# Optimization experiments

Hardware: AMD Instinct MI355X
Metric: run time of the kernel (lower is better)

Reference implementation:

```python
import jax, jax.numpy as jnp
import numpy as np
from jax import lax

WEIGHT_BITS = 8
ACT_BITS = 8
EPS = 1e-8


def ste_round(x):
    # straight-through estimator round
    return x + lax.stop_gradient(jnp.round(x) - x)


def fq_sym(x, bits=WEIGHT_BITS):
    # symmetric per-tensor signed fake quant (Brevitas Int*PerTensorFloat style)
    n = 2.0 ** (bits - 1) - 1.0
    scale = lax.stop_gradient(jnp.maximum(jnp.max(jnp.abs(x)), EPS) / n)
    return jnp.clip(ste_round(x / scale), -n, n) * scale


def quant_relu(x, bits=ACT_BITS):
    # QuantReLU: relu then unsigned per-tensor fake quant
    n = 2.0 ** bits - 1.0
    y = jax.nn.relu(x)
    scale = lax.stop_gradient(jnp.maximum(jnp.max(y), EPS) / n)
    return jnp.clip(ste_round(y / scale), 0.0, n) * scale


def qconv(x, w, b, groups=1):
    # QuantConv2d: fake-quant weights & bias, then conv (stride 1, same padding)
    pad = w.shape[-1] // 2
    wq = fq_sym(w, WEIGHT_BITS)
    bq = fq_sym(b, WEIGHT_BITS)
    y = lax.conv_general_dilated(
        x, wq, window_strides=(1, 1), padding=[(pad, pad), (pad, pad)],
        dimension_numbers=('NCHW', 'OIHW', 'NCHW'), feature_group_count=groups)
    return y + bq[None, :, None, None]


def residual_dw(x, w, b):
    # Residual(depthwise conv -> QuantReLU) with QuantIdentity(ActQuant) on both branches
    C = x.shape[1]
    h = quant_relu(qconv(x, w, b, groups=C))
    return fq_sym(h, ACT_BITS) + fq_sym(x, ACT_BITS)


def setup_inputs() -> dict:
    key = jax.random.key(0)
    ks = jax.random.split(key, 11)
    B, C, H, W = 8, 128, 128, 128
    CO = 256
    s = 0.05
    return {
        'x': jax.random.normal(ks[0], (B, C, H, W), jnp.float32),
        'dw1_w': jax.random.normal(ks[1], (C, 1, 3, 3), jnp.float32) * s,
        'dw1_b': jax.random.normal(ks[2], (C,), jnp.float32) * s,
        'dw2_w': jax.random.normal(ks[3], (C, 1, 3, 3), jnp.float32) * s,
        'dw2_b': jax.random.normal(ks[4], (C,), jnp.float32) * s,
        'pw1_w': jax.random.normal(ks[5], (4 * C, C, 1, 1), jnp.float32) * s,
        'pw1_b': jax.random.normal(ks[6], (4 * C,), jnp.float32) * s,
        'pw2_w': jax.random.normal(ks[7], (C, 4 * C, 1, 1), jnp.float32) * s,
        'pw2_b': jax.random.normal(ks[8], (C,), jnp.float32) * s,
        'up_w': jax.random.normal(ks[9], (CO, C, 3, 3), jnp.float32) * s,
        'up_b': jax.random.normal(ks[10], (CO,), jnp.float32) * s,
    }


def reference(x, dw1_w, dw1_b, dw2_w, dw2_b, pw1_w, pw1_b, pw2_w, pw2_b, up_w, up_b):
    # depth=1 block
    h = residual_dw(x, dw1_w, dw1_b)
    h = residual_dw(h, dw2_w, dw2_b)
    h = quant_relu(qconv(h, pw1_w, pw1_b))       # 1x1 expand C -> 4C
    h = quant_relu(qconv(h, pw2_w, pw2_b))       # 1x1 contract 4C -> C
    h = quant_relu(qconv(h, up_w, up_b))         # ConvBlock 3x3 C -> ch_out
    return h
```

## Files before the change

### kernel.cpp

```cpp
#include <hip/hip_runtime.h>

#define EPSQ 1e-8f

typedef unsigned short u16;
typedef signed char i8;
typedef __attribute__((ext_vector_type(4))) int int4v;
typedef __attribute__((ext_vector_type(4))) unsigned int uint4v;

static constexpr int  Bn = 8, Cc = 128, Hh = 128, Ww = 128, HW = Hh * Ww;
static constexpr int  C4 = 512, CO = 256;
static constexpr long NX   = (long)Bn * Cc * HW;
static constexpr long NOUT = (long)Bn * CO * HW;

#define MFMAI8(a,b,c) __builtin_amdgcn_mfma_i32_16x16x64_i8(a,b,c,0,0,0)

__device__ __forceinline__ float ubits(unsigned u) { return __uint_as_float(u); }


__device__ __forceinline__ void block_max_atomic(float v, unsigned* slot) {
    #pragma unroll
    for (int off = 32; off; off >>= 1) v = fmaxf(v, __shfl_down(v, off));
    __shared__ float sm[8];
    int lane = threadIdx.x & 63, wid = threadIdx.x >> 6;
    if (lane == 0) sm[wid] = v;
    __syncthreads();
    if (threadIdx.x == 0) {
        float m = sm[0];
        int nw = (blockDim.x + 63) >> 6;
        for (int i = 1; i < nw; i++) m = fmaxf(m, sm[i]);
        if (m > __uint_as_float(*(volatile unsigned*)slot))
            atomicMax(slot, __float_as_uint(m));
    }
    __syncthreads();
}

__device__ __forceinline__ void block_max_atomic2(float v, unsigned* slot, float* sm) {
    #pragma unroll
    for (int off = 32; off; off >>= 1) v = fmaxf(v, __shfl_down(v, off));
    int lane = threadIdx.x & 63, wid = threadIdx.x >> 6;
    __syncthreads();
    if (lane == 0) sm[wid] = v;
    __syncthreads();
    if (threadIdx.x == 0) {
        float m = sm[0];
        int nw = (blockDim.x + 63) >> 6;
        for (int i = 1; i < nw; i++) m = fmaxf(m, sm[i]);
        if (m > __uint_as_float(*(volatile unsigned*)slot))
            atomicMax(slot, __float_as_uint(m));
    }
}


__global__ void absmax_kernel(const float* __restrict__ x, long n, unsigned* slot) {
    long i = (long)blockIdx.x * blockDim.x + threadIdx.x;
    long stride = (long)gridDim.x * blockDim.x;
    const float4* x4 = (const float4*)x;
    long n4 = n >> 2;
    float m = 0.f;
    for (long j = i; j < n4; j += stride) {
        float4 v = x4[j];
        m = fmaxf(m, fmaxf(fmaxf(fabsf(v.x), fabsf(v.y)), fmaxf(fabsf(v.z), fabsf(v.w))));
    }
    block_max_atomic(m, slot);
}

struct QW { const float* src; float* dstF; i8* dstC; int n; int mode; int slot; int kdim; };

__device__ __forceinline__ QW qw_select(const QW& q0, const QW& q1, const QW& q2, const QW& q3,
                                        const QW& q4, const QW& q5, const QW& q6, const QW& q7,
                                        const QW& q8, const QW& q9, int t) {
    switch (t) {
        case 0: return q0; case 1: return q1; case 2: return q2; case 3: return q3;
        case 4: return q4; case 5: return q5; case 6: return q6; case 7: return q7;
        case 8: return q8; default: return q9;
    }
}

__global__ void wabsmax_kernel(QW q0, QW q1, QW q2, QW q3, QW q4,
                               QW q5, QW q6, QW q7, QW q8, QW q9,
                               unsigned* __restrict__ scal) {
    QW q = qw_select(q0, q1, q2, q3, q4, q5, q6, q7, q8, q9, blockIdx.y);
    int i0 = blockIdx.x * blockDim.x + threadIdx.x;
    int str = gridDim.x * blockDim.x;
    float m = 0.f;
    for (int i = i0; i < q.n; i += str) m = fmaxf(m, fabsf(q.src[i]));
    block_max_atomic(m, scal + 16 + blockIdx.y);
}

__global__ void wquant_kernel(QW q0, QW q1, QW q2, QW q3, QW q4,
                              QW q5, QW q6, QW q7, QW q8, QW q9,
                              unsigned* __restrict__ scal) {
    QW q = qw_select(q0, q1, q2, q3, q4, q5, q6, q7, q8, q9, blockIdx.y);
    float s = fmaxf(ubits(scal[16 + blockIdx.y]), EPSQ) / 127.f;
    if (q.mode != 0 && blockIdx.x == 0 && threadIdx.x == 0) scal[q.slot] = __float_as_uint(s);
    int i0 = blockIdx.x * blockDim.x + threadIdx.x;
    int str = gridDim.x * blockDim.x;
    for (int i = i0; i < q.n; i += str) {
        float v = fminf(fmaxf(rintf(q.src[i] / s), -127.f), 127.f);
        int code = (int)v;
        if (q.mode == 0) q.dstF[i] = v * s;
        else if (q.mode == 1) {
            int o = i / q.kdim, k = i % q.kdim;
            int otile = o >> 4, r = o & 15, kb = k >> 6, qq = (k & 63) >> 4, e = k & 15;
            q.dstC[((otile * (q.kdim >> 6) + kb) * 64 + qq * 16 + r) * 16 + e] = (i8)code;
        } else {
            int o = i / 1152, rem = i % 1152, c = rem / 9, t = rem % 9;
            int otile = o >> 4, r = o & 15, kb = c >> 6, qq = (c & 63) >> 4, e = c & 15;
            q.dstC[(((otile * 9 + t) * 2 + kb) * 64 + qq * 16 + r) * 16 + e] = (i8)code;
        }
    }
}


__global__ void corr_kernel(const float* __restrict__ pw2_w, const float* __restrict__ up_w,
                            const unsigned* __restrict__ scal,
                            int* __restrict__ corrP2, int* __restrict__ corrU) {
    int lane = threadIdx.x;
    if (blockIdx.y == 0) {
        int o = blockIdx.x;
        if (o >= 128) return;
        float s = fmaxf(ubits(scal[16 + 6]), EPSQ) / 127.f;
        int sum = 0;
        for (int k = lane; k < 512; k += 64)
            sum += (int)fminf(fmaxf(rintf(pw2_w[o * 512 + k] / s), -127.f), 127.f);
        #pragma unroll
        for (int off = 32; off; off >>= 1) sum += __shfl_down(sum, off);
        if (lane == 0) corrP2[o] = sum;
    } else {
        int o = blockIdx.x;
        float s = fmaxf(ubits(scal[16 + 8]), EPSQ) / 127.f;
        int sum[3] = {0, 0, 0};
        for (int i = lane; i < 1152; i += 64) {
            int t = i % 9;
            int code = (int)fminf(fmaxf(rintf(up_w[o * 1152 + i] / s), -127.f), 127.f);
            sum[t / 3] += code;
        }
        #pragma unroll
        for (int r = 0; r < 3; r++) {
            int v = sum[r];
            #pragma unroll
            for (int off = 32; off; off >>= 1) v += __shfl_down(v, off);
            if (lane == 0) corrU[r * 256 + o] = v;
        }
    }
}


__global__ void dwconv_kernel(const float* __restrict__ in, const float* __restrict__ wq,
                              const float* __restrict__ bq, float* __restrict__ out,
                              unsigned* mslot) {
    int bc = blockIdx.x;
    int c  = bc & (Cc - 1);
    float w[9];
    #pragma unroll
    for (int k = 0; k < 9; k++) w[k] = wq[c * 9 + k];
    float bias = bq[c];
    const float* src = in + (long)bc * HW;
    float* dst = out + (long)bc * HW;
    int j  = threadIdx.x & (Ww - 1);
    int r2 = threadIdx.x >> 7;
    float mm = 0.f;
    #pragma unroll
    for (int rr = 0; rr < 4; rr++) {
        int i = blockIdx.y * 8 + rr * 2 + r2;
        float acc = 0.f;
        #pragma unroll
        for (int di = 0; di < 3; di++) {
            int ii = i + di - 1;
            if (ii < 0 || ii >= Hh) continue;
            #pragma unroll
            for (int dj = 0; dj < 3; dj++) {
                int jj = j + dj - 1;
                if (jj < 0 || jj >= Ww) continue;
                acc = fmaf(w[di * 3 + dj], src[ii * Ww + jj], acc);
            }
        }
        acc += bias;
        dst[i * Ww + j] = acc;
        mm = fmaxf(mm, fmaxf(acc, 0.f));
    }
    block_max_atomic(mm, mslot);
}


__global__ void residual_kernel(const float4* __restrict__ t, const float4* __restrict__ xin,
                                float4* __restrict__ r, const unsigned* __restrict__ scal,
                                int mReluIdx, int mXIdx, unsigned* mOut) {
    float s1  = fmaxf(__uint_as_float(scal[mReluIdx]), EPSQ) / 255.f;
    float mh  = 255.f * s1;
    float s1b = fmaxf(mh, EPSQ) / 127.f;
    float sx  = fmaxf(__uint_as_float(scal[mXIdx]), EPSQ) / 127.f;
    long i0 = (long)blockIdx.x * blockDim.x + threadIdx.x;
    long str = (long)gridDim.x * blockDim.x;
    long n4 = NX >> 2;
    float mm = 0.f;
    for (long i = i0; i < n4; i += str) {
        float4 tv = t[i];
        float4 xv = xin[i];
        float o[4];
        float tc[4] = {tv.x, tv.y, tv.z, tv.w};
        float xc[4] = {xv.x, xv.y, xv.z, xv.w};
        #pragma unroll
        for (int k = 0; k < 4; k++) {
            float h  = fminf(rintf(fmaxf(tc[k], 0.f) / s1), 255.f) * s1;
            float hq = fminf(fmaxf(rintf(h / s1b), -127.f), 127.f) * s1b;
            float xq = fminf(fmaxf(rintf(xc[k] / sx), -127.f), 127.f) * sx;
            o[k] = hq + xq;
            mm = fmaxf(mm, fabsf(o[k]));
        }
        float4 ov = {o[0], o[1], o[2], o[3]};
        r[i] = ov;
    }
    if (mOut) block_max_atomic(mm, mOut);
}


__global__ __launch_bounds__(256) void residual2_codes_kernel(
    const float* __restrict__ t2, const float* __restrict__ r1,
    i8* __restrict__ jc, i8* __restrict__ ic, const unsigned* __restrict__ scal) {
    float s1  = fmaxf(ubits(scal[3]), EPSQ) / 255.f;
    float s1b = fmaxf(255.f * s1, EPSQ) / 127.f;
    float sx  = fmaxf(ubits(scal[2]), EPSQ) / 127.f;
    int b = blockIdx.x >> 8;
    long px0 = (long)(blockIdx.x & 255) * 64;
    __shared__ __align__(16) i8 lj[64 * 128];
    __shared__ __align__(16) i8 li[64 * 128];
    int px = threadIdx.x & 63, cq = threadIdx.x >> 6;
    for (int it = 0; it < 8; it++) {
        int cb = it * 16 + cq * 4;
        unsigned pj = 0, pi = 0;
        #pragma unroll
        for (int e = 0; e < 4; e++) {
            int c = cb + e;
            long g = ((long)b * Cc + c) * HW + px0 + px;
            float t = t2[g], x = r1[g];
            float hq = fminf(rintf(fmaxf(t, 0.f) / s1), 255.f) * s1;
            int j = (int)fminf(fmaxf(rintf(hq / s1b), -127.f), 127.f);
            int i = (int)fminf(fmaxf(rintf(x / sx), -127.f), 127.f);
            pj |= ((unsigned)(unsigned char)(i8)j) << (8 * e);
            pi |= ((unsigned)(unsigned char)(i8)i) << (8 * e);
        }
        int ad = (px * 128 + cb) ^ ((px & 7) << 4);
        *reinterpret_cast<int*>(lj + ad) = (int)pj;
        *reinterpret_cast<int*>(li + ad) = (int)pi;
    }
    __syncthreads();
    for (int s = threadIdx.x; s < 512; s += 256) {
        int px2 = s >> 3, sl = s & 7;
        int ad = (px2 * 128 + sl * 16) ^ ((px2 & 7) << 4);
        long dst = ((long)b * HW + px0 + px2) * 128 + sl * 16;
        *reinterpret_cast<uint4v*>(jc + dst) = *reinterpret_cast<uint4v*>(lj + ad);
        *reinterpret_cast<uint4v*>(ic + dst) = *reinterpret_cast<uint4v*>(li + ad);
    }
}

template<int K, int OB, bool DUAL, int MODE>
__global__ __launch_bounds__(256) void pwmfma_kernel(
    const i8* __restrict__ bc0, const i8* __restrict__ bc1,
    const i8* __restrict__ wc, const float* __restrict__ bias,
    i8* __restrict__ outc, const unsigned* __restrict__ scal,
    const int* __restrict__ corrI,
    int O_total, int sInSlot, int sWSlot, int sOutSlot, unsigned* mslot) {

    constexpr int F = OB / 64;
    constexpr int KB = K / 64;
    constexpr int LSZ = (DUAL ? 2 : 1) * 64 * K;
    __shared__ __align__(16) i8 lds[LSZ];
    int lane = threadIdx.x & 63, wv = threadIdx.x >> 6;
    int lane15 = lane & 15;
    int b = blockIdx.x >> 8;
    long px0 = (long)(blockIdx.x & 255) * 64;
    long pixbase = (long)b * HW + px0;
    int oB = blockIdx.y * OB;
    int oW = wv * (OB / 4);

    for (int s = threadIdx.x; s < 4 * K; s += 256) {
        int px = s / (K / 16), cs = s % (K / 16);
        long gsrc = (pixbase + px) * K + cs * 16;
        int addr = (px * K + cs * 16) ^ ((px & 7) << 4);
        *reinterpret_cast<uint4v*>(lds + addr) = *reinterpret_cast<const uint4v*>(bc0 + gsrc);
        if (DUAL)
            *reinterpret_cast<uint4v*>(lds + 64 * K + addr) =
                *reinterpret_cast<const uint4v*>(bc1 + gsrc);
    }
    __syncthreads();

    const int4v z4 = {0, 0, 0, 0};
    int4v accA[F][4], accB[F][4];
    #pragma unroll
    for (int i = 0; i < F; i++)
        #pragma unroll
        for (int j = 0; j < 4; j++) { accA[i][j] = z4; accB[i][j] = z4; }

    const i8* wpack = wc + ((long)((oB + oW) >> 4) * KB) * 1024 + lane * 16;

    #pragma unroll
    for (int kb = 0; kb < KB; kb++) {
        int4v a[F];
        #pragma unroll
        for (int f = 0; f < F; f++)
            a[f] = *reinterpret_cast<const int4v*>(wpack + ((long)f * KB + kb) * 1024);
        #pragma unroll
        for (int fn = 0; fn < 4; fn++) {
            int col = fn * 16 + lane15;
            int ad = (col * K + kb * 64 + (lane >> 4) * 16) ^ ((col & 7) << 4);
            int4v b0 = *reinterpret_cast<const int4v*>(lds + ad);
            #pragma unroll
            for (int f = 0; f < F; f++) accA[f][fn] = MFMAI8(a[f], b0, accA[f][fn]);
            if (DUAL) {
                int4v b1 = *reinterpret_cast<const int4v*>(lds + 64 * K + ad);
                #pragma unroll
                for (int f = 0; f < F; f++) accB[f][fn] = MFMAI8(a[f], b1, accB[f][fn]);
            }
        }
    }

    float sW = ubits(scal[sWSlot]);
    float sA, sB_;
    if (DUAL) {
        float s1 = fmaxf(ubits(scal[3]), EPSQ) / 255.f;
        sA  = fmaxf(255.f * s1, EPSQ) / 127.f;
        sB_ = fmaxf(ubits(scal[2]), EPSQ) / 127.f;
    } else {
        sA = fmaxf(ubits(scal[sInSlot]), EPSQ) / 255.f;
        sB_ = 0.f;
    }

    if (MODE == 0) {
        float mm = 0.f;
        #pragma unroll
        for (int f = 0; f < F; f++)
        #pragma unroll
        for (int fn = 0; fn < 4; fn++)
        #pragma unroll
        for (int r = 0; r < 4; r++) {
            int o = oB + oW + f * 16 + (lane >> 4) * 4 + r;
            float av;
            if (DUAL) av = sA * (float)accA[f][fn][r] + sB_ * (float)accB[f][fn][r];
            else      av = sA * (float)(accA[f][fn][r] + (corrI[o] << 7));
            float v = fmaxf(sW * av + bias[o], 0.f);
            mm = fmaxf(mm, v);
        }
        block_max_atomic2(mm, mslot, reinterpret_cast<float*>(lds));
    } else {
        float sOut = fmaxf(ubits(scal[sOutSlot]), EPSQ) / 255.f;
        __syncthreads();
        #pragma unroll
        for (int f = 0; f < F; f++)
        #pragma unroll
        for (int fn = 0; fn < 4; fn++) {
            int orow0 = oW + f * 16 + (lane >> 4) * 4;
            unsigned pk = 0;
            #pragma unroll
            for (int r = 0; r < 4; r++) {
                int o = oB + orow0 + r;
                float av;
                if (DUAL) av = sA * (float)accA[f][fn][r] + sB_ * (float)accB[f][fn][r];
                else      av = sA * (float)(accA[f][fn][r] + (corrI[o] << 7));
                float v = fmaxf(sW * av + bias[o], 0.f);
                int code = (int)fminf(rintf(v / sOut), 255.f) - 128;
                pk |= ((unsigned)(unsigned char)(i8)code) << (8 * r);
            }
            int pxl = fn * 16 + lane15;
            int ad = (pxl * OB + orow0) ^ ((pxl & 7) << 4);
            *reinterpret_cast<int*>(lds + ad) = (int)pk;
        }
        __syncthreads();
        constexpr int CH = OB / 16;
        for (int s = threadIdx.x; s < 64 * CH; s += 256) {
            int px = s / CH, sl = s % CH;
            int ad = (px * OB + sl * 16) ^ ((px & 7) << 4);
            *reinterpret_cast<uint4v*>(outc + (pixbase + px) * O_total + oB + sl * 16) =
                *reinterpret_cast<uint4v*>(lds + ad);
        }
    }
}


__global__ __launch_bounds__(256) void conv3x3_mfma_kernel(
    const i8* __restrict__ xc,
    const i8* __restrict__ wc,
    const float* __restrict__ bias, float* __restrict__ out,
    const unsigned* __restrict__ scal, const int* __restrict__ corrU,
    unsigned* mslot) {

    __shared__ __align__(16) i8 lds[3 * 66 * 128];
    int lane = threadIdx.x & 63, wv = threadIdx.x >> 6;
    int lane15 = lane & 15;
    int bx = blockIdx.x;
    int b = bx >> 8, h = (bx >> 1) & 127, wseg = bx & 1;
    int oW = wv * 64;

    for (int s = threadIdx.x; s < 3 * 66 * 8; s += 256) {
        int row = s / (66 * 8), rem = s % (66 * 8), col = rem >> 3, sl = rem & 7;
        int hh = h + row - 1;
        if (hh < 0 || hh > 127) continue;
        int wgl = wseg * 64 + col - 1;
        uint4v v = {0x80808080u, 0x80808080u, 0x80808080u, 0x80808080u};
        if (wgl >= 0 && wgl <= 127) {
            long pix = (long)b * HW + (long)hh * 128 + wgl;
            v = *reinterpret_cast<const uint4v*>(xc + pix * 128 + sl * 16);
        }
        int addr = ((row * 66 + col) * 128 + sl * 16) ^ ((col & 7) << 4);
        *reinterpret_cast<uint4v*>(lds + addr) = v;
    }
    __syncthreads();

    const int4v z4 = {0, 0, 0, 0};
    int4v acc[4][4];
    #pragma unroll
    for (int i = 0; i < 4; i++)
        #pragma unroll
        for (int j = 0; j < 4; j++) acc[i][j] = z4;

    const i8* wpack = wc + (long)(wv * 4) * 18 * 1024 + lane * 16;
    for (int di = 0; di < 3; di++) {
        int hh = h + di - 1;
        if (hh < 0 || hh > 127) continue;
        for (int dj = 0; dj < 3; dj++) {
            int tap = di * 3 + dj;
            #pragma unroll
            for (int kb = 0; kb < 2; kb++) {
                int4v a[4];
                #pragma unroll
                for (int f = 0; f < 4; f++)
                    a[f] = *reinterpret_cast<const int4v*>(
                        wpack + ((long)(f * 9 + tap) * 2 + kb) * 1024);
                int4v bb[4];
                #pragma unroll
                for (int fn = 0; fn < 4; fn++) {
                    int col = fn * 16 + lane15 + dj;
                    bb[fn] = *reinterpret_cast<const int4v*>(lds +
                        (((di * 66 + col) * 128 + kb * 64 + (lane >> 4) * 16) ^ ((col & 7) << 4)));
                }
                #pragma unroll
                for (int f = 0; f < 4; f++)
                    #pragma unroll
                    for (int fn = 0; fn < 4; fn++)
                        acc[f][fn] = MFMAI8(a[f], bb[fn], acc[f][fn]);
            }
        }
    }

    float s5 = fmaxf(ubits(scal[5]), EPSQ) / 255.f;
    float sc = ubits(scal[10]) * s5;
    float mm = 0.f;
    #pragma unroll
    for (int f = 0; f < 4; f++)
    #pragma unroll
    for (int r = 0; r < 4; r++) {
        int o = oW + f * 16 + (lane >> 4) * 4 + r;
        int csum = corrU[256 + o];
        if (h > 0)   csum += corrU[o];
        if (h < 127) csum += corrU[512 + o];
        #pragma unroll
        for (int fn = 0; fn < 4; fn++) {
            int px = wseg * 64 + fn * 16 + lane15;
            int ai = acc[f][fn][r] + (csum << 7);
            float v = fmaxf(sc * (float)ai + bias[o], 0.f);
            mm = fmaxf(mm, v);
            out[((long)(b * CO + o)) * HW + h * 128 + px] = v;
        }
    }
    block_max_atomic2(mm, mslot, reinterpret_cast<float*>(lds));
}


__global__ void quant_inplace_kernel(float4* __restrict__ p, long n4,
                                     const unsigned* __restrict__ scal, int idx) {
    float s = fmaxf(__uint_as_float(scal[idx]), EPSQ) / 255.f;
    long i0 = (long)blockIdx.x * blockDim.x + threadIdx.x;
    long str = (long)gridDim.x * blockDim.x;
    for (long i = i0; i < n4; i += str) {
        float4 v = p[i];
        v.x = fminf(rintf(v.x / s), 255.f) * s;
        v.y = fminf(rintf(v.y / s), 255.f) * s;
        v.z = fminf(rintf(v.z / s), 255.f) * s;
        v.w = fminf(rintf(v.w / s), 255.f) * s;
        p[i] = v;
    }
}


extern "C" void kernel_launch(void* const* d_in, const int* in_sizes, int n_in,
                              void* d_out, int out_size, void* d_ws, size_t ws_size,
                              hipStream_t stream) {
    (void)in_sizes; (void)n_in; (void)out_size; (void)ws_size;
    const float* x     = (const float*)d_in[0];
    const float* dw1_w = (const float*)d_in[1];
    const float* dw1_b = (const float*)d_in[2];
    const float* dw2_w = (const float*)d_in[3];
    const float* dw2_b = (const float*)d_in[4];
    const float* pw1_w = (const float*)d_in[5];
    const float* pw1_b = (const float*)d_in[6];
    const float* pw2_w = (const float*)d_in[7];
    const float* pw2_b = (const float*)d_in[8];
    const float* up_w  = (const float*)d_in[9];
    const float* up_b  = (const float*)d_in[10];
    float* out = (float*)d_out;
    float* ws  = (float*)d_ws;

    float* Abuf = ws;
    float* Bbuf = ws + NX;
    i8*    jcode   = (i8*)(ws + 2 * NX);
    i8*    icode   = jcode + NX;
    i8*    p1codes = (i8*)ws;
    i8*    p2codes = (i8*)(ws + 2 * NX);

    float* wbase  = ws + 3 * NX;
    float* wq_dw1 = wbase;          float* bq_dw1 = wbase + 1152;
    float* wq_dw2 = wbase + 1280;   float* bq_dw2 = wbase + 2432;
    float* bq_pw1 = wbase + 2560;
    float* bq_pw2 = wbase + 3072;
    float* bq_up  = wbase + 3200;
    i8*    wc_pw1 = (i8*)(wbase + 3456);
    i8*    wc_pw2 = (i8*)(wbase + 19840);
    i8*    wc_up  = (i8*)(wbase + 36224);
    unsigned* scal = (unsigned*)(wbase + 109952);
    int*   corrU  = (int*)(wbase + 109984);
    int*   corrP2 = (int*)(wbase + 110752);

    (void)hipMemsetAsync(scal, 0, 32 * sizeof(unsigned), stream);

    QW q0{dw1_w, wq_dw1, nullptr, 1152, 0, 0, 9},
       q1{dw1_b, bq_dw1, nullptr, 128, 0, 0, 1},
       q2{dw2_w, wq_dw2, nullptr, 1152, 0, 0, 9},
       q3{dw2_b, bq_dw2, nullptr, 128, 0, 0, 1},
       q4{pw1_w, nullptr, wc_pw1, 65536, 1, 8, 128},
       q5{pw1_b, bq_pw1, nullptr, 512, 0, 0, 1},
       q6{pw2_w, nullptr, wc_pw2, 65536, 1, 9, 512},
       q7{pw2_b, bq_pw2, nullptr, 128, 0, 0, 1},
       q8{up_w, nullptr, wc_up, 294912, 2, 10, 128},
       q9{up_b, bq_up, nullptr, 256, 0, 0, 1};
    wabsmax_kernel<<<dim3(32, 10), 256, 0, stream>>>(q0, q1, q2, q3, q4, q5, q6, q7, q8, q9, scal);
    wquant_kernel<<<dim3(32, 10), 256, 0, stream>>>(q0, q1, q2, q3, q4, q5, q6, q7, q8, q9, scal);
    corr_kernel<<<dim3(256, 2), 64, 0, stream>>>(pw2_w, up_w, scal, corrP2, corrU);

    absmax_kernel<<<2048, 256, 0, stream>>>(x, NX, scal + 0);

    dwconv_kernel<<<dim3(Bn * Cc, Hh / 8), 256, 0, stream>>>(x, wq_dw1, bq_dw1, Abuf, scal + 1);
    residual_kernel<<<4096, 256, 0, stream>>>((const float4*)Abuf, (const float4*)x,
                                              (float4*)Bbuf, scal, 1, 0, scal + 2);
    dwconv_kernel<<<dim3(Bn * Cc, Hh / 8), 256, 0, stream>>>(Bbuf, wq_dw2, bq_dw2, Abuf, scal + 3);
    residual2_codes_kernel<<<2048, 256, 0, stream>>>(Abuf, Bbuf, jcode, icode, scal);

    pwmfma_kernel<128, 256, true, 0><<<dim3(2048, 2), 256, 0, stream>>>(
        jcode, icode, wc_pw1, bq_pw1, nullptr, scal, nullptr, C4, 0, 8, 0, scal + 4);
    pwmfma_kernel<128, 256, true, 1><<<dim3(2048, 2), 256, 0, stream>>>(
        jcode, icode, wc_pw1, bq_pw1, p1codes, scal, nullptr, C4, 0, 8, 4, nullptr);

    pwmfma_kernel<512, 128, false, 0><<<dim3(2048, 1), 256, 0, stream>>>(
        p1codes, nullptr, wc_pw2, bq_pw2, nullptr, scal, corrP2, Cc, 4, 9, 0, scal + 5);
    pwmfma_kernel<512, 128, false, 1><<<dim3(2048, 1), 256, 0, stream>>>(
        p1codes, nullptr, wc_pw2, bq_pw2, p2codes, scal, corrP2, Cc, 4, 9, 5, nullptr);

    conv3x3_mfma_kernel<<<2048, 256, 0, stream>>>(p2codes, wc_up, bq_up, out, scal, corrU, scal + 6);
    quant_inplace_kernel<<<4096, 256, 0, stream>>>((float4*)out, NOUT / 4, scal, 6);
}
```

Before: 571.4 us.

## Fuse input absmax into first dwconv and vectorize dwconv with float4 rows

Removes the separate absmax pass over x by computing the absolute max of the input inside the first depthwise conv kernel, which already reads x. The depthwise conv is rewritten so each thread produces 4 adjacent outputs for 2 rows from float4 loads of 4 input rows, building shifted vectors from neighbouring float4s. This saves one full read of the input tensor and cuts per-element load instructions. It adds a second block reduction and relies on the interior rows each block reads covering all of x.

After: 523.4 us. 8.4% less time.

```diff
diff --git a/kernel.cpp b/kernel.cpp
--- a/kernel.cpp
+++ b/kernel.cpp
@@ -15,6 +15,13 @@
 #define MFMAI8(a,b,c) __builtin_amdgcn_mfma_i32_16x16x64_i8(a,b,c,0,0,0)
 
 __device__ __forceinline__ float ubits(unsigned u) { return __uint_as_float(u); }
+
+__device__ __forceinline__ float4 fma4(float a, float4 b, float4 c) {
+    float4 r;
+    r.x = fmaf(a, b.x, c.x); r.y = fmaf(a, b.y, c.y);
+    r.z = fmaf(a, b.z, c.z); r.w = fmaf(a, b.w, c.w);
+    return r;
+}
 
 
 __device__ __forceinline__ void block_max_atomic(float v, unsigned* slot) {
@@ -48,20 +55,6 @@
         if (m > __uint_as_float(*(volatile unsigned*)slot))
             atomicMax(slot, __float_as_uint(m));
     }
-}
-
-
-__global__ void absmax_kernel(const float* __restrict__ x, long n, unsigned* slot) {
-    long i = (long)blockIdx.x * blockDim.x + threadIdx.x;
-    long stride = (long)gridDim.x * blockDim.x;
-    const float4* x4 = (const float4*)x;
-    long n4 = n >> 2;
-    float m = 0.f;
-    for (long j = i; j < n4; j += stride) {
-        float4 v = x4[j];
-        m = fmaxf(m, fmaxf(fmaxf(fabsf(v.x), fabsf(v.y)), fmaxf(fabsf(v.z), fabsf(v.w))));
-    }
-    block_max_atomic(m, slot);
 }
 
 struct QW { const float* src; float* dstF; i8* dstC; int n; int mode; int slot; int kdim; };
@@ -146,9 +139,10 @@
 }
 
 
-__global__ void dwconv_kernel(const float* __restrict__ in, const float* __restrict__ wq,
-                              const float* __restrict__ bq, float* __restrict__ out,
-                              unsigned* mslot) {
+__global__ __launch_bounds__(256) void dwconv_kernel(
+    const float* __restrict__ in, const float* __restrict__ wq,
+    const float* __restrict__ bq, float* __restrict__ out,
+    unsigned* mslot, unsigned* xslot) {
     int bc = blockIdx.x;
     int c  = bc & (Cc - 1);
     float w[9];
@@ -157,29 +151,45 @@
     float bias = bq[c];
     const float* src = in + (long)bc * HW;
     float* dst = out + (long)bc * HW;
-    int j  = threadIdx.x & (Ww - 1);
-    int r2 = threadIdx.x >> 7;
+    int tg = threadIdx.x & 31;
+    int rh = threadIdx.x >> 5;
+    int j0 = tg * 4;
+    int r0 = blockIdx.y * 16 + rh * 2;
+
+    const float4 z4 = {0.f, 0.f, 0.f, 0.f};
+    float4 L[4], C[4], R[4];
+    float mx = 0.f;
+    #pragma unroll
+    for (int t = 0; t < 4; t++) {
+        int row = r0 - 1 + t;
+        if (row < 0 || row > 127) { L[t] = z4; C[t] = z4; R[t] = z4; continue; }
+        const float* p = src + row * Ww + j0;
+        float4 cv = *reinterpret_cast<const float4*>(p);
+        C[t] = cv;
+        L[t] = (j0 > 0)   ? *reinterpret_cast<const float4*>(p - 4) : z4;
+        R[t] = (j0 < 124) ? *reinterpret_cast<const float4*>(p + 4) : z4;
+        mx = fmaxf(mx, fmaxf(fmaxf(fabsf(cv.x), fabsf(cv.y)),
+                             fmaxf(fabsf(cv.z), fabsf(cv.w))));
+    }
+
     float mm = 0.f;
     #pragma unroll
-    for (int rr = 0; rr < 4; rr++) {
-        int i = blockIdx.y * 8 + rr * 2 + r2;
-        float acc = 0.f;
-        #pragma unroll
-        for (int di = 0; di < 3; di++) {
-            int ii = i + di - 1;
-            if (ii < 0 || ii >= Hh) continue;
-            #pragma unroll
-            for (int dj = 0; dj < 3; dj++) {
-                int jj = j + dj - 1;
-                if (jj < 0 || jj >= Ww) continue;
-                acc = fmaf(w[di * 3 + dj], src[ii * Ww + jj], acc);
-            }
-        }
-        acc += bias;
-        dst[i * Ww + j] = acc;
-        mm = fmaxf(mm, fmaxf(acc, 0.f));
-    }
-    block_max_atomic(mm, mslot);
+    for (int rr = 0; rr < 2; rr++) {
+        float4 acc = {bias, bias, bias, bias};
+        #pragma unroll
+        for (int t = 0; t < 3; t++) {
+            float4 l = L[rr + t], cc = C[rr + t], r = R[rr + t];
+            float4 wm1 = {l.w, cc.x, cc.y, cc.z};
+            float4 wp1 = {cc.y, cc.z, cc.w, r.x};
+            acc = fma4(w[t * 3 + 0], wm1, acc);
+            acc = fma4(w[t * 3 + 1], cc,  acc);
+            acc = fma4(w[t * 3 + 2], wp1, acc);
+        }
+        *reinterpret_cast<float4*>(dst + (r0 + rr) * Ww + j0) = acc;
+        mm = fmaxf(mm, fmaxf(fmaxf(acc.x, acc.y), fmaxf(acc.z, acc.w)));
+    }
+    block_max_atomic(fmaxf(mm, 0.f), mslot);
+    if (xslot) block_max_atomic(mx, xslot);
 }
 
 
@@ -536,12 +546,12 @@
     wquant_kernel<<<dim3(32, 10), 256, 0, stream>>>(q0, q1, q2, q3, q4, q5, q6, q7, q8, q9, scal);
     corr_kernel<<<dim3(256, 2), 64, 0, stream>>>(pw2_w, up_w, scal, corrP2, corrU);
 
-    absmax_kernel<<<2048, 256, 0, stream>>>(x, NX, scal + 0);
-
-    dwconv_kernel<<<dim3(Bn * Cc, Hh / 8), 256, 0, stream>>>(x, wq_dw1, bq_dw1, Abuf, scal + 1);
+    dwconv_kernel<<<dim3(Bn * Cc, Hh / 16), 256, 0, stream>>>(x, wq_dw1, bq_dw1, Abuf,
+                                                              scal + 1, scal + 0);
     residual_kernel<<<4096, 256, 0, stream>>>((const float4*)Abuf, (const float4*)x,
                                               (float4*)Bbuf, scal, 1, 0, scal + 2);
-    dwconv_kernel<<<dim3(Bn * Cc, Hh / 8), 256, 0, stream>>>(Bbuf, wq_dw2, bq_dw2, Abuf, scal + 3);
+    dwconv_kernel<<<dim3(Bn * Cc, Hh / 16), 256, 0, stream>>>(Bbuf, wq_dw2, bq_dw2, Abuf,
+                                                              scal + 3, nullptr);
     residual2_codes_kernel<<<2048, 256, 0, stream>>>(Abuf, Bbuf, jcode, icode, scal);
 
     pwmfma_kernel<128, 256, true, 0><<<dim3(2048, 2), 256, 0, stream>>>(
```
